# Kernel optimization log

Hardware: AMD Instinct MI355X
Metric: run time of the kernel (lower is better)

The kernel has to match this reference:

```python
import jax, jax.numpy as jnp
import numpy as np

T, B = 512, 256
OBS, FEAT, H, ACT = 128, 512, 256, 16
LOG2PI = float(np.log(2.0 * np.pi))


def layer_norm(x, w, b, eps=1e-5):
    m = x.mean(-1, keepdims=True)
    v = ((x - m) ** 2).mean(-1, keepdims=True)
    return (x - m) / jnp.sqrt(v + eps) * w + b


def mlp_features(x, W1, b1, W2, b2, gw, gb):
    h = jax.nn.relu(x @ W1.T + b1)
    h = layer_norm(h @ W2.T + b2, gw, gb)
    return jax.nn.relu(h)


def masked_lstm_scan(feat, done, h0, c0, Wih, Whh, bih, bhh):
    # feat: [T,B,H], done: [T,B] float, h0/c0: [B,H]. PyTorch gate order i,f,g,o.
    def step(carry, inp):
        h, c = carry
        x, d = inp
        m = (1.0 - d)[:, None]
        h = h * m
        c = c * m
        g = x @ Wih.T + bih + h @ Whh.T + bhh
        i, f, gg, o = jnp.split(g, 4, axis=-1)
        c = jax.nn.sigmoid(f) * c + jax.nn.sigmoid(i) * jnp.tanh(gg)
        h = jax.nn.sigmoid(o) * jnp.tanh(c)
        return (h, c), h
    (hT, cT), hs = jax.lax.scan(step, (h0, c0), (feat, done))
    return hs, hT, cT


def setup_inputs():
    key = jax.random.key(0)
    ks = jax.random.split(key, 40)
    rn = lambda k, s, sc=0.05: jax.random.normal(k, s, dtype=jnp.float32) * sc
    inp = {}
    inp["x"] = jax.random.normal(ks[0], (T * B, OBS), dtype=jnp.float32)
    inp["done"] = jax.random.randint(ks[1], (T * B,), 0, 2).astype(jnp.int32)
    inp["actor_h0"] = rn(ks[2], (1, B, H), 0.1)
    inp["actor_c0"] = rn(ks[3], (1, B, H), 0.1)
    inp["critic_h0"] = rn(ks[4], (1, B, H), 0.1)
    inp["critic_c0"] = rn(ks[5], (1, B, H), 0.1)
    inp["action"] = jax.random.normal(ks[6], (T * B, ACT), dtype=jnp.float32)
    j = 7
    for p in ("a", "c"):
        inp[p + "_W1"] = rn(ks[j], (FEAT, OBS)); j += 1
        inp[p + "_b1"] = jnp.zeros((FEAT,), jnp.float32)
        inp[p + "_W2"] = rn(ks[j], (H, FEAT)); j += 1
        inp[p + "_b2"] = jnp.zeros((H,), jnp.float32)
        inp[p + "_flnw"] = jnp.ones((H,), jnp.float32)
        inp[p + "_flnb"] = jnp.zeros((H,), jnp.float32)
        inp[p + "_Wih"] = rn(ks[j], (4 * H, H)); j += 1
        inp[p + "_Whh"] = rn(ks[j], (4 * H, H)); j += 1
        inp[p + "_bih"] = jnp.zeros((4 * H,), jnp.float32)
        inp[p + "_bhh"] = jnp.zeros((4 * H,), jnp.float32)
        inp[p + "_lnw"] = jnp.ones((H,), jnp.float32)
        inp[p + "_lnb"] = jnp.zeros((H,), jnp.float32)
    inp["a_mW"] = rn(ks[j], (ACT, H)); j += 1
    inp["a_mb"] = jnp.zeros((ACT,), jnp.float32)
    inp["a_logstd"] = jnp.zeros((1, ACT), jnp.float32)
    inp["c_hW"] = rn(ks[j], (1, H)); j += 1
    inp["c_hb"] = jnp.zeros((1,), jnp.float32)
    return inp


def reference(x, done, actor_h0, actor_c0, critic_h0, critic_c0, action,
              a_W1, a_b1, a_W2, a_b2, a_flnw, a_flnb, a_Wih, a_Whh, a_bih, a_bhh,
              a_lnw, a_lnb, a_mW, a_mb, a_logstd,
              c_W1, c_b1, c_W2, c_b2, c_flnw, c_flnb, c_Wih, c_Whh, c_bih, c_bhh,
              c_lnw, c_lnb, c_hW, c_hb):
    Bn = actor_h0.shape[1]
    N = x.shape[0]
    Tn = N // Bn
    d = done.astype(jnp.float32).reshape(Tn, Bn)
    # actor branch
    a_feat = mlp_features(x, a_W1, a_b1, a_W2, a_b2, a_flnw, a_flnb).reshape(Tn, Bn, -1)
    hs, ah, acell = masked_lstm_scan(a_feat, d, actor_h0[0], actor_c0[0], a_Wih, a_Whh, a_bih, a_bhh)
    ha = layer_norm(hs.reshape(N, -1), a_lnw, a_lnb)
    mean = ha @ a_mW.T + a_mb
    logstd = jnp.broadcast_to(a_logstd, mean.shape)
    std = jnp.exp(logstd)
    logprob = (-0.5 * ((action - mean) / std) ** 2 - logstd - 0.5 * LOG2PI).sum(1)
    entropy = (0.5 + 0.5 * LOG2PI + logstd).sum(1)
    # critic branch
    c_feat = mlp_features(x, c_W1, c_b1, c_W2, c_b2, c_flnw, c_flnb).reshape(Tn, Bn, -1)
    cs, ch, ccell = masked_lstm_scan(c_feat, d, critic_h0[0], critic_c0[0], c_Wih, c_Whh, c_bih, c_bhh)
    hc = layer_norm(cs.reshape(N, -1), c_lnw, c_lnb)
    value = hc @ c_hW.T + c_hb
    return (logprob, entropy, value, ah[None], acell[None], ch[None], ccell[None])
```

## Files before the change

### kernel.cpp

```cpp
#include <hip/hip_runtime.h>

typedef unsigned short u16;
typedef unsigned long long u64;
typedef __attribute__((ext_vector_type(8))) short short8;
typedef __attribute__((ext_vector_type(4))) float floatx4;
typedef __attribute__((ext_vector_type(4))) float f32x4;
typedef __attribute__((ext_vector_type(4))) int intx4;

#define LOG2PI_F 1.8378770664093453f
#define LOG2E_F 1.4426950408889634f
#define TWOLOG2E_F 2.8853900817779268f

__device__ inline float bf2f(u16 u) { return __uint_as_float(((unsigned)u) << 16); }
__device__ inline u16 f2bf(float f) {
  unsigned u = __float_as_uint(f);
  u += 0x7fff + ((u >> 16) & 1);
  return (u16)(u >> 16);
}

struct PrepArgs {
  const float* src[18];
  const float* src2[18];
  void* dst[18];
  int mode[18];
  int n[18];
  int blk0[19];
  int nseg;
};

__global__ __launch_bounds__(256) void k_prep(PrepArgs a) {
  int b = blockIdx.x, s = 0;
  while (s + 1 < a.nseg && b >= a.blk0[s + 1]) ++s;
  int i = (b - a.blk0[s]) * 1024 + threadIdx.x * 4;
  if (i >= a.n[s]) return;
  if (a.mode[s] == 0) {
    f32x4 v = *(const f32x4*)(a.src[s] + i);
    u64 p = (u64)f2bf(v[0]) | ((u64)f2bf(v[1]) << 16)
          | ((u64)f2bf(v[2]) << 32) | ((u64)f2bf(v[3]) << 48);
    *(u64*)((u16*)a.dst[s] + i) = p;
  } else if (a.mode[s] == 1) {
    f32x4 x = *(const f32x4*)(a.src[s] + i);
    f32x4 y = *(const f32x4*)(a.src2[s] + i);
    *(f32x4*)((float*)a.dst[s] + i) = x + y;
  } else {
    *(f32x4*)((float*)a.dst[s] + i) = *(const f32x4*)(a.src[s] + i);
  }
}

__global__ __launch_bounds__(256) void k_quant(const float* __restrict__ w0,
                                               const float* __restrict__ w1,
                                               char* __restrict__ q, float* __restrict__ sr) {
  int tid = threadIdx.x, lane = tid & 63;
  int row = blockIdx.x * 4 + (tid >> 6);
  int br = row >> 10, r = row & 1023;
  const float* src = (br ? w1 : w0) + (size_t)r * 256 + lane * 4;
  f32x4 v = *(const f32x4*)src;
  float m = fmaxf(fmaxf(fabsf(v[0]), fabsf(v[1])), fmaxf(fabsf(v[2]), fabsf(v[3])));
#pragma unroll
  for (int o = 32; o >= 1; o >>= 1) m = fmaxf(m, __shfl_xor(m, o));
  float inv = m > 0.f ? 127.f / m : 0.f;
  int pk = 0;
#pragma unroll
  for (int c = 0; c < 4; ++c) {
    int qq = __float2int_rn(v[c] * inv);
    qq = qq > 127 ? 127 : (qq < -127 ? -127 : qq);
    pk |= (qq & 255) << (8 * c);
  }
  *(int*)(q + (size_t)row * 256 + lane * 4) = pk;
  if (lane == 0) {
    float sf = (r >= 512 && r < 768) ? TWOLOG2E_F : -LOG2E_F;
    sr[row] = m * (1.f / (127.f * 127.f)) * sf;
  }
}

template <int EPI, int AF32>
__global__ __launch_bounds__(256, 2) void k_gemm(
    const void* __restrict__ Agv, const u16* __restrict__ Wg,
    const float* __restrict__ biasP, void* __restrict__ outv,
    int Nn, int K, int relu, int Tseg,
    long az, long wz, long oz) {
  __shared__ u16 As[128][72];
  __shared__ u16 Ws[128][72];
  const int tid = threadIdx.x;
  const int z = blockIdx.z;
  const int bn = blockIdx.x * 128;
  const int bm = blockIdx.y * 128;
  const int w = tid >> 6, lane = tid & 63, lm = lane & 15, lq = lane >> 4;
  const int wr = (w >> 1) * 64, wc = (w & 1) * 64;
  const int tr = tid >> 3, tc = (tid & 7) * 8;

  const u16* Ab = (const u16*)Agv;
  const float* Af = (const float*)Agv;
  const u16* Wb = Wg + (size_t)z * wz;

  floatx4 acc[4][4] = {};

  for (int k0 = 0; k0 < K; k0 += 64) {
    __syncthreads();
#pragma unroll
    for (int rr = 0; rr < 4; ++rr) {
      int row = rr * 32 + tr;
      if (AF32) {
        const float* src = Af + (size_t)z * az + (size_t)(bm + row) * K + k0 + tc;
        f32x4 v0 = *(const f32x4*)src;
        f32x4 v1 = *(const f32x4*)(src + 4);
        short8 sv;
#pragma unroll
        for (int c = 0; c < 4; ++c) { sv[c] = (short)f2bf(v0[c]); sv[4 + c] = (short)f2bf(v1[c]); }
        *(short8*)&As[row][tc] = sv;
      } else {
        *(short8*)&As[row][tc] = *(const short8*)(Ab + (size_t)z * az + (size_t)(bm + row) * K + k0 + tc);
      }
      *(short8*)&Ws[row][tc] = *(const short8*)(Wb + (size_t)(bn + row) * K + k0 + tc);
    }
    __syncthreads();
#pragma unroll
    for (int kk = 0; kk < 2; ++kk) {
      short8 a4[4], b4[4];
#pragma unroll
      for (int i = 0; i < 4; ++i) {
        a4[i] = *(const short8*)&As[wr + i * 16 + lm][kk * 32 + lq * 8];
        b4[i] = *(const short8*)&Ws[wc + i * 16 + lm][kk * 32 + lq * 8];
      }
#pragma unroll
      for (int i = 0; i < 4; ++i)
#pragma unroll
        for (int j = 0; j < 4; ++j)
          acc[i][j] = __builtin_amdgcn_mfma_f32_16x16x32_bf16(a4[i], b4[j], acc[i][j], 0, 0, 0);
    }
  }

#pragma unroll
  for (int i = 0; i < 4; ++i) {
#pragma unroll
    for (int j = 0; j < 4; ++j) {
      int col = bn + wc + j * 16 + lm;
      float bv = biasP[(size_t)z * Nn + col];
      float v[4];
#pragma unroll
      for (int r = 0; r < 4; ++r) {
        float t = acc[i][j][r] + bv;
        v[r] = relu ? fmaxf(t, 0.f) : t;
      }
      int row0l = bm + wr + i * 16 + lq * 4;
      if (EPI == 1) {
        u16* o = (u16*)outv + (size_t)z * oz;
#pragma unroll
        for (int r = 0; r < 4; ++r) o[(size_t)(row0l + r) * Nn + col] = f2bf(v[r]);
      } else {
        float s = (col >= 512 && col < 768) ? TWOLOG2E_F : -LOG2E_F;
        int t_l = row0l >> 8;
        int bfull = row0l & 255;
        int bbx = bfull >> 4;
        int mq = (bfull >> 2) & 3;
        u64 p = (u64)f2bf(v[0] * s) | ((u64)f2bf(v[1] * s) << 16)
              | ((u64)f2bf(v[2] * s) << 32) | ((u64)f2bf(v[3] * s) << 48);
        u16* o = (u16*)outv + (size_t)z * oz;
        size_t idx = ((((size_t)bbx * Tseg + t_l) * 4 + mq) * 1024 + col) * 4;
        *(u64*)(o + idx) = p;
      }
    }
  }
}

__global__ __launch_bounds__(256) void k_ln_relu(const u16* __restrict__ in,
                                                 const float* __restrict__ lnp,
                                                 u16* __restrict__ out,
                                                 long inz, long outz) {
  int z = blockIdx.y;
  int w = threadIdx.x >> 6, lane = threadIdx.x & 63;
  size_t row = (size_t)blockIdx.x * 4 + w;
  const u16* ip = in + (size_t)z * inz;
  u16* op = out + (size_t)z * outz;
  const float* gw = lnp + (size_t)z * 512;
  const float* gb = gw + 256;
  u64 hv = *(const u64*)(ip + row * 256 + lane * 4);
  float x[4];
#pragma unroll
  for (int c = 0; c < 4; ++c) x[c] = bf2f((u16)(hv >> (16 * c)));
  float s = x[0] + x[1] + x[2] + x[3];
  float q = x[0] * x[0] + x[1] * x[1] + x[2] * x[2] + x[3] * x[3];
#pragma unroll
  for (int o = 32; o >= 1; o >>= 1) { s += __shfl_xor(s, o); q += __shfl_xor(q, o); }
  float mean = s * (1.f / 256.f);
  float var = q * (1.f / 256.f) - mean * mean;
  float rs = rsqrtf(var + 1e-5f);
  u64 p = 0;
#pragma unroll
  for (int c = 0; c < 4; ++c) {
    int k = lane * 4 + c;
    float y = (x[c] - mean) * rs * gw[k] + gb[k];
    y = fmaxf(y, 0.f);
    p |= ((u64)f2bf(y)) << (16 * c);
  }
  *(u64*)(op + row * 256 + lane * 4) = p;
}

struct ScanArgs {
  const u16 *gin0, *gin1;
  const char *whq0, *whq1;
  const float *sr0, *sr1;
  const float *h00, *h01, *c00, *c01;
  char *hs0, *hs1;
  float *hsv0, *hsv1, *csv0, *csv1;
  const int* done;
  int t0, Tseg;
};

__global__ __launch_bounds__(512, 2) void k_scan(ScanArgs A) {
  const int bb = blockIdx.x & 127, br = blockIdx.x >> 7;
  const int bbx = bb >> 3;
  const int rb = bb << 1;
  const int tid = threadIdx.x;
  const int w = tid >> 6, lane = tid & 63, lm = lane & 15, lq = lane >> 4;
  const int bsel = lq & 1;
  const int mrow = lane >> 5;
  const int jj = w * 32 + bsel * 16 + lm;
  const int hoff = (jj >> 4) * 256 + mrow * 16 + (jj & 15);

  extern __shared__ char dsm[];
  char* hl = dsm;

  const char* whq = br ? A.whq1 : A.whq0;
  const float* srP = br ? A.sr1 : A.sr0;
  const u16* gin = (br ? A.gin1 : A.gin0) + (size_t)bbx * A.Tseg * 16384;
  const float* h0 = br ? A.h01 : A.h00;
  const float* c0 = br ? A.c01 : A.c00;
  char* hs = (br ? A.hs1 : A.hs0) + bbx * 4096;
  float* hsv = br ? A.hsv1 : A.hsv0;
  float* csv = br ? A.csv1 : A.csv0;

  intx4 wreg[8][4];
#pragma unroll
  for (int g = 0; g < 4; ++g)
#pragma unroll
    for (int b2 = 0; b2 < 2; ++b2)
#pragma unroll
      for (int kk = 0; kk < 4; ++kk)
        wreg[g * 2 + b2][kk] =
            *(const intx4*)(whq + (size_t)(g * 256 + w * 32 + b2 * 16 + lm) * 256 + kk * 64 + lq * 16);

  float srw[4];
#pragma unroll
  for (int g = 0; g < 4; ++g) srw[g] = srP[g * 256 + jj];

  float creg = c0[(size_t)(rb + mrow) * 256 + jj];

  {
    int c = tid & 255, buf = tid >> 8;
    int kk = c >> 6, lqk = (c >> 4) & 3, m = c & 15;
    intx4 val = {0, 0, 0, 0};
    if (buf == 0 && m < 2) {
      const float* hp = h0 + (size_t)(rb + m) * 256 + kk * 64 + lqk * 16;
#pragma unroll
      for (int q4 = 0; q4 < 4; ++q4) {
        int pk = 0;
#pragma unroll
        for (int b = 0; b < 4; ++b) {
          int qv = __float2int_rn(hp[q4 * 4 + b] * 127.f);
          qv = qv > 127 ? 127 : (qv < -127 ? -127 : qv);
          pk |= (qv & 255) << (8 * b);
        }
        val[q4] = pk;
      }
    }
    *(intx4*)&hl[buf * 4096 + c * 16] = val;
  }
  __syncthreads();

  const int goff = ((rb >> 2) & 3) * 4096 + (rb & 3) + mrow;

  u16 gnxt[4];
#pragma unroll
  for (int g = 0; g < 4; ++g)
    gnxt[g] = gin[(size_t)(g * 256 + jj) * 4 + goff];
  int daN = A.done[(size_t)A.t0 * 256 + rb + (lm & 1)];
  int dcN = A.done[(size_t)A.t0 * 256 + rb + mrow];

  intx4 z4 = {0, 0, 0, 0};

  for (int tl = 0; tl < A.Tseg; ++tl) {
    const int curo = (tl & 1) * 4096, nxto = curo ^ 4096;

    u16 gcur[4];
#pragma unroll
    for (int g = 0; g < 4; ++g) gcur[g] = gnxt[g];
    int da = daN;
    int dc = dcN;

    if (tl + 1 < A.Tseg) {
#pragma unroll
      for (int g = 0; g < 4; ++g)
        gnxt[g] = gin[(size_t)(tl + 1) * 16384 + (size_t)(g * 256 + jj) * 4 + goff];
      int tn = A.t0 + tl + 1;
      daN = A.done[(size_t)tn * 256 + rb + (lm & 1)];
      dcN = A.done[(size_t)tn * 256 + rb + mrow];
    }

    intx4 af[4];
#pragma unroll
    for (int kk = 0; kk < 4; ++kk) {
      intx4 hv = *(const intx4*)&hl[curo + kk * 1024 + lane * 16];
      af[kk] = da ? z4 : hv;
    }

    intx4 acc[8] = {};
#pragma unroll
    for (int kk = 0; kk < 4; ++kk)
#pragma unroll
      for (int a = 0; a < 8; ++a)
        acc[a] = __builtin_amdgcn_mfma_i32_16x16x64_i8(af[kk], wreg[a][kk], acc[a], 0, 0, 0);

    float av[4];
#pragma unroll
    for (int g = 0; g < 4; ++g) {
      int s00 = __shfl(acc[2 * g][0], lm);
      int s01 = __shfl(acc[2 * g][1], lm);
      int s10 = __shfl(acc[2 * g + 1][0], lm);
      int s11 = __shfl(acc[2 * g + 1][1], lm);
      int sel = bsel ? (mrow ? s11 : s10) : (mrow ? s01 : s00);
      av[g] = (float)sel;
    }

    {
      float cprev = dc ? 0.f : creg;
      float xi = fmaf(av[0], srw[0], bf2f(gcur[0]));
      float xf = fmaf(av[1], srw[1], bf2f(gcur[1]));
      float xg = fmaf(av[2], srw[2], bf2f(gcur[2]));
      float xo = fmaf(av[3], srw[3], bf2f(gcur[3]));
      float ig = __builtin_amdgcn_rcpf(1.f + __builtin_amdgcn_exp2f(xi));
      float fg = __builtin_amdgcn_rcpf(1.f + __builtin_amdgcn_exp2f(xf));
      float gg = 1.f - 2.f * __builtin_amdgcn_rcpf(1.f + __builtin_amdgcn_exp2f(xg));
      float og = __builtin_amdgcn_rcpf(1.f + __builtin_amdgcn_exp2f(xo));
      float cn = fg * cprev + ig * gg;
      creg = cn;
      float th = 1.f - 2.f * __builtin_amdgcn_rcpf(1.f + __builtin_amdgcn_exp2f(TWOLOG2E_F * cn));
      float hn = og * th;
      int qv = __float2int_rn(hn * 127.f);
      hl[nxto + hoff] = (char)qv;
      if (tl == A.Tseg - 1) {
        size_t idx = (size_t)(rb + mrow) * 256 + jj;
        hsv[idx] = hn;
        csv[idx] = cn;
      }
    }
    asm volatile("s_waitcnt lgkmcnt(0)" ::: "memory");
    __builtin_amdgcn_s_barrier();
    __builtin_amdgcn_sched_barrier(0);
    if (tid < 128) {
      int a_l = nxto + (tid >> 3) * 256 + (tid & 7) * 4;
      int mg = (bb & 7) * 2 + ((tid >> 2) & 1);
      int a_g = (tid >> 3) * 256 + mg * 16 + (tid & 3) * 4;
      *(int*)(hs + (size_t)tl * 65536 + a_g) = *(const int*)&hl[a_l];
    }
  }
}

__global__ __launch_bounds__(256) void k_head(
    const char* __restrict__ hs_a, const char* __restrict__ hs_c,
    const float* __restrict__ a_lnw, const float* __restrict__ a_lnb,
    const float* __restrict__ c_lnw, const float* __restrict__ c_lnb,
    const float* __restrict__ mW, const float* __restrict__ mb,
    const float* __restrict__ logstd, const float* __restrict__ hW,
    const float* __restrict__ hb, const float* __restrict__ action,
    float* __restrict__ lp, float* __restrict__ ent, float* __restrict__ val,
    int row0) {
  __shared__ float smW[16][260];
  __shared__ float shW[256];
  __shared__ float spar[4][256];
  __shared__ float hrow[4][264];
  int tid = threadIdx.x;
  for (int i = tid; i < 4096; i += 256) smW[i >> 8][i & 255] = mW[i];
  shW[tid] = hW[tid];
  spar[0][tid] = a_lnw[tid]; spar[1][tid] = a_lnb[tid];
  spar[2][tid] = c_lnw[tid]; spar[3][tid] = c_lnb[tid];
  __syncthreads();

  int w = tid >> 6, lane = tid & 63, lm = lane & 15, lq = lane >> 4;
  float entc = 0.f;
#pragma unroll
  for (int j = 0; j < 16; ++j) entc += 0.5f + 0.5f * LOG2PI_F + logstd[j];
  float ls = logstd[lm];
  float sd = __expf(ls);
  float mbj = mb[lm];

  int rbase = (blockIdx.x * 4 + w) * 16;
  for (int rr = 0; rr < 16; ++rr) {
    int row = rbase + rr;
    int m = row & 15;
    size_t base = (size_t)(row >> 8) * 65536 + (size_t)((row >> 4) & 15) * 4096;
    int off = (lane >> 4) * 1024 + (m + 16 * ((lane >> 2) & 3)) * 16 + (lane & 3) * 4;
    int va = *(const int*)(hs_a + base + off);
    float x[4];
#pragma unroll
    for (int c = 0; c < 4; ++c) x[c] = (float)((va << (24 - 8 * c)) >> 24) * (1.f / 127.f);
    float s = x[0] + x[1] + x[2] + x[3];
    float q = x[0] * x[0] + x[1] * x[1] + x[2] * x[2] + x[3] * x[3];
#pragma unroll
    for (int o = 32; o >= 1; o >>= 1) { s += __shfl_xor(s, o); q += __shfl_xor(q, o); }
    float mean = s * (1.f / 256.f);
    float rs = rsqrtf(q * (1.f / 256.f) - mean * mean + 1e-5f);
    floatx4 hh;
#pragma unroll
    for (int c = 0; c < 4; ++c) {
      int k = lane * 4 + c;
      hh[c] = (x[c] - mean) * rs * spar[0][k] + spar[1][k];
    }
    *(floatx4*)&hrow[w][lane * 4] = hh;
    float p = 0.f;
#pragma unroll 16
    for (int k2 = 0; k2 < 64; ++k2) {
      int kx = lq * 64 + ((k2 + lq * 16) & 63);
      p = fmaf(hrow[w][kx], smW[lm][kx], p);
    }
    p += __shfl_xor(p, 16);
    p += __shfl_xor(p, 32);
    float meanj = p + mbj;
    float aj = action[(size_t)(row0 + row) * 16 + lm];
    float z = (aj - meanj) / sd;
    float term = -0.5f * z * z - ls - 0.5f * LOG2PI_F;
    term += __shfl_xor(term, 1);
    term += __shfl_xor(term, 2);
    term += __shfl_xor(term, 4);
    term += __shfl_xor(term, 8);
    int vc = *(const int*)(hs_c + base + off);
    float y[4];
#pragma unroll
    for (int c = 0; c < 4; ++c) y[c] = (float)((vc << (24 - 8 * c)) >> 24) * (1.f / 127.f);
    float s2 = y[0] + y[1] + y[2] + y[3];
    float q2 = y[0] * y[0] + y[1] * y[1] + y[2] * y[2] + y[3] * y[3];
#pragma unroll
    for (int o = 32; o >= 1; o >>= 1) { s2 += __shfl_xor(s2, o); q2 += __shfl_xor(q2, o); }
    float mean2 = s2 * (1.f / 256.f);
    float rs2 = rsqrtf(q2 * (1.f / 256.f) - mean2 * mean2 + 1e-5f);
    float pv = 0.f;
#pragma unroll
    for (int c = 0; c < 4; ++c) {
      int k = lane * 4 + c;
      float hc = (y[c] - mean2) * rs2 * spar[2][k] + spar[3][k];
      pv = fmaf(hc, shW[k], pv);
    }
#pragma unroll
    for (int o = 32; o >= 1; o >>= 1) pv += __shfl_xor(pv, o);
    if (lane == 0) {
      lp[row0 + row] = term;
      ent[row0 + row] = entc;
      val[row0 + row] = pv + hb[0];
    }
  }
}

extern "C" void kernel_launch(void* const* d_in, const int* in_sizes, int n_in,
                              void* d_out, int out_size, void* d_ws, size_t ws_size,
                              hipStream_t stream) {
  const int N = 131072, T = 512;
  const float* x = (const float*)d_in[0];
  const int* done = (const int*)d_in[1];
  const float* h0i[2] = {(const float*)d_in[2], (const float*)d_in[4]};
  const float* c0i[2] = {(const float*)d_in[3], (const float*)d_in[5]};
  const float* action = (const float*)d_in[6];
  const float *W1[2], *b1[2], *W2[2], *b2[2], *flnw[2], *flnb[2];
  const float *Wih[2], *Whh[2], *bih[2], *bhh[2], *lnw[2], *lnb[2];
  for (int br = 0; br < 2; ++br) {
    int o = 7 + br * 12;
    W1[br] = (const float*)d_in[o + 0];  b1[br] = (const float*)d_in[o + 1];
    W2[br] = (const float*)d_in[o + 2];  b2[br] = (const float*)d_in[o + 3];
    flnw[br] = (const float*)d_in[o + 4]; flnb[br] = (const float*)d_in[o + 5];
    Wih[br] = (const float*)d_in[o + 6]; Whh[br] = (const float*)d_in[o + 7];
    bih[br] = (const float*)d_in[o + 8]; bhh[br] = (const float*)d_in[o + 9];
    lnw[br] = (const float*)d_in[o + 10]; lnb[br] = (const float*)d_in[o + 11];
  }
  const float* mW = (const float*)d_in[31];
  const float* mb = (const float*)d_in[32];
  const float* logstd = (const float*)d_in[33];
  const float* hW = (const float*)d_in[34];
  const float* hb = (const float*)d_in[35];

  float* out = (float*)d_out;
  float* o_lp = out;
  float* o_ent = out + N;
  float* o_val = out + 2 * N;
  float* o_ah = out + 3 * N;
  float* o_ac = o_ah + 65536;
  float* o_ch = o_ac + 65536;
  float* o_cc = o_ch + 65536;

  auto rq = [&](long sr2, long st2) -> size_t {
    long Ts = T / st2, Ms = N / sr2;
    size_t s = 0;
    auto al = [&](size_t b) { s += (b + 255) & ~(size_t)255; };
    al(2 * 65536 * 2); al(2 * 131072 * 2); al(2 * 262144 * 2);
    al(2 * 262144); al(2048 * 4);
    al(2 * 1024 * 4); al(2 * 512 * 4); al(2 * 256 * 4); al(1024 * 4);
    al(2 * 65536 * 4); al(2 * 65536 * 4);
    al((size_t)2 * Ms * 512 * 2);
    al((size_t)2 * Ms * 256 * 2);
    al((size_t)2 * N * 256 * 2);
    al((size_t)2 * Ts * 262144 * 2);
    al((size_t)2 * Ts * 65536);
    return s;
  };
  int sr = 16, st = 16;
  const int cand[7][2] = {{1, 1}, {2, 2}, {4, 4}, {4, 8}, {8, 8}, {8, 16}, {16, 16}};
  for (int i = 0; i < 7; ++i)
    if (rq(cand[i][0], cand[i][1]) + ((size_t)4 << 20) <= ws_size) { sr = cand[i][0]; st = cand[i][1]; break; }
  const long Ts = T / st, Ms = N / sr;

  char* pp = (char*)d_ws;
  auto carve = [&](size_t b) -> void* { void* r = pp; pp += (b + 255) & ~(size_t)255; return r; };
  u16* W1b = (u16*)carve(2 * 65536 * 2);
  u16* W2b = (u16*)carve(2 * 131072 * 2);
  u16* Wihb = (u16*)carve(2 * 262144 * 2);
  char* whhq = (char*)carve(2 * 262144);
  float* srowP = (float*)carve(2048 * 4);
  float* bihh = (float*)carve(2 * 1024 * 4);
  float* b1c = (float*)carve(2 * 512 * 4);
  float* b2c = (float*)carve(2 * 256 * 4);
  float* lnp = (float*)carve(1024 * 4);
  float* hsv = (float*)carve(2 * 65536 * 4);
  float* csv = (float*)carve(2 * 65536 * 4);
  u16* h1 = (u16*)carve((size_t)2 * Ms * 512 * 2);
  u16* g2 = (u16*)carve((size_t)2 * Ms * 256 * 2);
  u16* featP = (u16*)carve((size_t)2 * N * 256 * 2);
  u16* ginP = (u16*)carve((size_t)2 * Ts * 262144 * 2);
  char* hsbP = (char*)carve((size_t)2 * Ts * 65536);

  PrepArgs pa{};
  int ns = 0, blk = 0;
  auto addseg = [&](const float* s1, const float* s2, void* d, int n, int mode) {
    pa.src[ns] = s1; pa.src2[ns] = s2; pa.dst[ns] = d; pa.mode[ns] = mode; pa.n[ns] = n;
    pa.blk0[ns] = blk; blk += (n + 1023) / 1024; ++ns;
  };
  for (int br = 0; br < 2; ++br) {
    addseg(W1[br], nullptr, W1b + br * 65536, 65536, 0);
    addseg(W2[br], nullptr, W2b + br * 131072, 131072, 0);
    addseg(Wih[br], nullptr, Wihb + br * 262144, 262144, 0);
    addseg(bih[br], bhh[br], bihh + br * 1024, 1024, 1);
    addseg(b1[br], nullptr, b1c + br * 512, 512, 2);
    addseg(b2[br], nullptr, b2c + br * 256, 256, 2);
    addseg(flnw[br], nullptr, lnp + br * 512, 256, 2);
    addseg(flnb[br], nullptr, lnp + br * 512 + 256, 256, 2);
  }
  pa.nseg = ns;
  pa.blk0[ns] = blk;
  k_prep<<<blk, 256, 0, stream>>>(pa);
  k_quant<<<512, 256, 0, stream>>>(Whh[0], Whh[1], whhq, srowP);

  for (int s = 0; s < sr; ++s) {
    k_gemm<1, 1><<<dim3(4, Ms / 128, 2), 256, 0, stream>>>(
        x + (size_t)s * Ms * 128, W1b, b1c, h1, 512, 128, 1, 0,
        0L, 65536L, (long)Ms * 512);
    k_gemm<1, 0><<<dim3(2, Ms / 128, 2), 256, 0, stream>>>(
        h1, W2b, b2c, g2, 256, 512, 0, 0,
        (long)Ms * 512, 131072L, (long)Ms * 256);
    k_ln_relu<<<dim3(Ms / 4, 2), 256, 0, stream>>>(
        g2, lnp, featP + (size_t)s * Ms * 256, (long)Ms * 256, (long)N * 256);
  }

  for (int s = 0; s < st; ++s) {
    long t0 = s * Ts;
    k_gemm<2, 0><<<dim3(8, Ts * 2, 2), 256, 0, stream>>>(
        featP + (size_t)t0 * 65536, Wihb, bihh, ginP, 1024, 256, 0, (int)Ts,
        (long)N * 256, 262144L, Ts * 262144L);
    ScanArgs sa;
    sa.gin0 = ginP; sa.gin1 = ginP + Ts * 262144;
    sa.whq0 = whhq; sa.whq1 = whhq + 262144;
    sa.sr0 = srowP; sa.sr1 = srowP + 1024;
    sa.h00 = s ? hsv : h0i[0]; sa.h01 = s ? hsv + 65536 : h0i[1];
    sa.c00 = s ? csv : c0i[0]; sa.c01 = s ? csv + 65536 : c0i[1];
    sa.hs0 = hsbP; sa.hs1 = hsbP + Ts * 65536;
    bool last = (s == st - 1);
    sa.hsv0 = last ? o_ah : hsv; sa.hsv1 = last ? o_ch : hsv + 65536;
    sa.csv0 = last ? o_ac : csv; sa.csv1 = last ? o_cc : csv + 65536;
    sa.done = done; sa.t0 = (int)t0; sa.Tseg = (int)Ts;
    k_scan<<<256, 512, 8192, stream>>>(sa);
    k_head<<<(int)(Ts * 256 / 64), 256, 0, stream>>>(
        hsbP, hsbP + Ts * 65536, lnw[0], lnb[0], lnw[1], lnb[1],
        mW, mb, logstd, hW, hb, action,
        o_lp, o_ent, o_val, (int)(t0 * 256));
  }
}
```

Before: 1.931 ms.

## Split LSTM scan work across 16 waves per block with fewer MFMAs each

```diff
diff --git a/kernel.cpp b/kernel.cpp
--- a/kernel.cpp
+++ b/kernel.cpp
@@ -207,16 +207,16 @@
   int t0, Tseg;
 };
 
-__global__ __launch_bounds__(512, 2) void k_scan(ScanArgs A) {
+__global__ __launch_bounds__(1024, 1) void k_scan(ScanArgs A) {
   const int bb = blockIdx.x & 127, br = blockIdx.x >> 7;
   const int bbx = bb >> 3;
   const int rb = bb << 1;
   const int tid = threadIdx.x;
   const int w = tid >> 6, lane = tid & 63, lm = lane & 15, lq = lane >> 4;
-  const int bsel = lq & 1;
-  const int mrow = lane >> 5;
-  const int jj = w * 32 + bsel * 16 + lm;
-  const int hoff = (jj >> 4) * 256 + mrow * 16 + (jj & 15);
+  const int mrow = lq & 1;
+  const bool iscell = lq < 2;
+  const int jj = w * 16 + lm;
+  const int hoff = w * 256 + mrow * 16 + lm;
 
   extern __shared__ char dsm[];
   char* hl = dsm;
@@ -230,15 +230,13 @@
   float* hsv = br ? A.hsv1 : A.hsv0;
   float* csv = br ? A.csv1 : A.csv0;
 
-  intx4 wreg[8][4];
+  intx4 wreg[4][4];
 #pragma unroll
   for (int g = 0; g < 4; ++g)
 #pragma unroll
-    for (int b2 = 0; b2 < 2; ++b2)
-#pragma unroll
-      for (int kk = 0; kk < 4; ++kk)
-        wreg[g * 2 + b2][kk] =
-            *(const intx4*)(whq + (size_t)(g * 256 + w * 32 + b2 * 16 + lm) * 256 + kk * 64 + lq * 16);
+    for (int kk = 0; kk < 4; ++kk)
+      wreg[g][kk] =
+          *(const intx4*)(whq + (size_t)(g * 256 + w * 16 + lm) * 256 + kk * 64 + lq * 16);
 
   float srw[4];
 #pragma unroll
@@ -246,7 +244,7 @@
 
   float creg = c0[(size_t)(rb + mrow) * 256 + jj];
 
-  {
+  if (tid < 512) {
     int c = tid & 255, buf = tid >> 8;
     int kk = c >> 6, lqk = (c >> 4) & 3, m = c & 15;
     intx4 val = {0, 0, 0, 0};
@@ -268,14 +266,18 @@
   }
   __syncthreads();
 
-  const int goff = ((rb >> 2) & 3) * 4096 + (rb & 3) + mrow;
-
-  u16 gnxt[4];
-#pragma unroll
-  for (int g = 0; g < 4; ++g)
-    gnxt[g] = gin[(size_t)(g * 256 + jj) * 4 + goff];
-  int daN = A.done[(size_t)A.t0 * 256 + rb + (lm & 1)];
-  int dcN = A.done[(size_t)A.t0 * 256 + rb + mrow];
+  const u16* ginT = gin + ((rb >> 2) & 3) * 4096 + (rb & 3) + mrow + jj * 4;
+  const int* dptrA = A.done + (size_t)A.t0 * 256 + rb + (lm & 1);
+  const int* dptrC = A.done + (size_t)A.t0 * 256 + rb + mrow;
+
+  u16 gnxt[4] = {0, 0, 0, 0};
+  int dcN = 0;
+  int daN = *dptrA;
+  if (iscell) {
+#pragma unroll
+    for (int g = 0; g < 4; ++g) gnxt[g] = ginT[g * 1024];
+    dcN = *dptrC;
+  }
 
   intx4 z4 = {0, 0, 0, 0};
 
@@ -289,12 +291,15 @@
     int dc = dcN;
 
     if (tl + 1 < A.Tseg) {
-#pragma unroll
-      for (int g = 0; g < 4; ++g)
-        gnxt[g] = gin[(size_t)(tl + 1) * 16384 + (size_t)(g * 256 + jj) * 4 + goff];
-      int tn = A.t0 + tl + 1;
-      daN = A.done[(size_t)tn * 256 + rb + (lm & 1)];
-      dcN = A.done[(size_t)tn * 256 + rb + mrow];
+      ginT += 16384;
+      dptrA += 256;
+      dptrC += 256;
+      daN = *dptrA;
+      if (iscell) {
+#pragma unroll
+        for (int g = 0; g < 4; ++g) gnxt[g] = ginT[g * 1024];
+        dcN = *dptrC;
+      }
     }
 
     intx4 af[4];
@@ -304,30 +309,27 @@
       af[kk] = da ? z4 : hv;
     }
 
-    intx4 acc[8] = {};
+    intx4 acc[4] = {};
 #pragma unroll
     for (int kk = 0; kk < 4; ++kk)
 #pragma unroll
-      for (int a = 0; a < 8; ++a)
-        acc[a] = __builtin_amdgcn_mfma_i32_16x16x64_i8(af[kk], wreg[a][kk], acc[a], 0, 0, 0);
-
-    float av[4];
+      for (int g = 0; g < 4; ++g)
+        acc[g] = __builtin_amdgcn_mfma_i32_16x16x64_i8(af[kk], wreg[g][kk], acc[g], 0, 0, 0);
+
+    int av[4];
 #pragma unroll
     for (int g = 0; g < 4; ++g) {
-      int s00 = __shfl(acc[2 * g][0], lm);
-      int s01 = __shfl(acc[2 * g][1], lm);
-      int s10 = __shfl(acc[2 * g + 1][0], lm);
-      int s11 = __shfl(acc[2 * g + 1][1], lm);
-      int sel = bsel ? (mrow ? s11 : s10) : (mrow ? s01 : s00);
-      av[g] = (float)sel;
-    }
-
-    {
+      int s0 = __shfl(acc[g][0], lm);
+      int s1 = __shfl(acc[g][1], lm);
+      av[g] = mrow ? s1 : s0;
+    }
+
+    if (iscell) {
       float cprev = dc ? 0.f : creg;
-      float xi = fmaf(av[0], srw[0], bf2f(gcur[0]));
-      float xf = fmaf(av[1], srw[1], bf2f(gcur[1]));
-      float xg = fmaf(av[2], srw[2], bf2f(gcur[2]));
-      float xo = fmaf(av[3], srw[3], bf2f(gcur[3]));
+      float xi = fmaf((float)av[0], srw[0], bf2f(gcur[0]));
+      float xf = fmaf((float)av[1], srw[1], bf2f(gcur[1]));
+      float xg = fmaf((float)av[2], srw[2], bf2f(gcur[2]));
+      float xo = fmaf((float)av[3], srw[3], bf2f(gcur[3]));
       float ig = __builtin_amdgcn_rcpf(1.f + __builtin_amdgcn_exp2f(xi));
       float fg = __builtin_amdgcn_rcpf(1.f + __builtin_amdgcn_exp2f(xf));
       float gg = 1.f - 2.f * __builtin_amdgcn_rcpf(1.f + __builtin_amdgcn_exp2f(xg));
@@ -573,7 +575,7 @@
     sa.hsv0 = last ? o_ah : hsv; sa.hsv1 = last ? o_ch : hsv + 65536;
     sa.csv0 = last ? o_ac : csv; sa.csv1 = last ? o_cc : csv + 65536;
     sa.done = done; sa.t0 = (int)t0; sa.Tseg = (int)Ts;
-    k_scan<<<256, 512, 8192, stream>>>(sa);
+    k_scan<<<256, 1024, 8192, stream>>>(sa);
     k_head<<<(int)(Ts * 256 / 64), 256, 0, stream>>>(
         hsbP, hsbP + Ts * 65536, lnw[0], lnb[0], lnw[1], lnb[1],
         mW, mb, logstd, hW, hb, action,
```

Result: no change. 1.933 ms (+0.1%).
